# Kernel optimization log

Hardware: AMD Instinct MI355X
Metric: run time of the kernel (lower is better)

The kernel has to match this reference:

```python
import jax, jax.numpy as jnp
import numpy as np
import math

IMAGE_SIZE = 256
VIEWING_ANGLE = 30.0  # degrees
NEAR = 0.1
FAR = 100.0
CHUNK = 50


def _look_at(vertices):
    # nr.look_at with at=origin, up=+y, eye from viewing_angle (as in __init__)
    eye = jnp.array([0.0, 0.0, -(1.0 / math.tan(math.radians(VIEWING_ANGLE)) + 1.0)],
                    dtype=vertices.dtype)
    at = jnp.zeros(3, dtype=vertices.dtype)
    up = jnp.array([0.0, 1.0, 0.0], dtype=vertices.dtype)
    z = at - eye
    z = z / jnp.linalg.norm(z)
    x = jnp.cross(up, z)
    x = x / jnp.linalg.norm(x)
    y = jnp.cross(z, x)
    y = y / jnp.linalg.norm(y)
    R = jnp.stack([x, y, z])  # [3,3] rows = camera axes
    return (vertices - eye) @ R.T


def _perspective(v):
    # nr.perspective: x,y divided by z*tan(angle); z (camera depth) kept
    width = math.tan(math.radians(VIEWING_ANGLE))
    z = v[..., 2]
    zs = jnp.where(jnp.abs(z) < 1e-5, 1e-5, z)  # avoid div-by-zero for behind-camera verts
    return jnp.stack([v[..., 0] / (zs * width), v[..., 1] / (zs * width), z], axis=-1)


def reference(vertices, faces):
    """Renderer.forward(vertices, faces, mode='depth'):
    fill_back -> look_at -> perspective -> vertices_to_faces -> rasterize_depth.
    Returns depth image [B, H, W] (FAR where no face covers the pixel)."""
    B = vertices.shape[0]
    # fill_back: append faces with reversed vertex order
    faces2 = jnp.concatenate([faces, faces[:, :, ::-1]], axis=1)  # [B, 2F, 3]
    v_scr = _perspective(_look_at(vertices))                      # [B, V, 3]
    # vertices_to_faces gather
    fv = jax.vmap(lambda v, f: v[f])(v_scr, faces2)               # [B, 2F, 3, 3]
    F2 = fv.shape[1]
    nsteps = F2 // CHUNK
    fv = fv.reshape(B, nsteps, CHUNK, 3, 3).transpose(1, 0, 2, 3, 4)  # [S,B,C,3,3]

    is_ = IMAGE_SIZE
    p = (2.0 * jnp.arange(is_, dtype=vertices.dtype) + 1.0 - is_) / is_  # pixel centers in (-1,1)
    py, px = jnp.meshgrid(p, p, indexing='ij')  # [H,W]

    def step(buf, f):  # f: [B,C,3,3]; z-buffer min over this face chunk
        x = f[..., 0][..., None, None]  # [B,C,3,1,1]
        y = f[..., 1][..., None, None]
        z = f[..., 2]                   # [B,C,3] camera-space depth per vertex
        x0, x1, x2 = x[:, :, 0], x[:, :, 1], x[:, :, 2]
        y0, y1, y2 = y[:, :, 0], y[:, :, 1], y[:, :, 2]
        area = (x1 - x0) * (y2 - y0) - (x2 - x0) * (y1 - y0)  # [B,C,1,1] signed 2*area
        area_s = jnp.where(jnp.abs(area) < 1e-8, 1e-8, area)
        # screen-space barycentric weights (edge functions / area)
        w0 = ((x1 - px) * (y2 - py) - (x2 - px) * (y1 - py)) / area_s
        w1 = ((x2 - px) * (y0 - py) - (x0 - px) * (y2 - py)) / area_s
        w2 = 1.0 - w0 - w1
        zc = jnp.maximum(z, 1e-4)  # safe for masked-out faces only
        # perspective-correct depth: z = 1 / (w0/z0 + w1/z1 + w2/z2)
        inv_z = (w0 / zc[:, :, 0, None, None] + w1 / zc[:, :, 1, None, None]
                 + w2 / zc[:, :, 2, None, None])
        zp = 1.0 / jnp.maximum(inv_z, 1e-6)
        front = jnp.all(z > NEAR, axis=-1)[..., None, None]
        inside = (w0 >= 0) & (w1 >= 0) & (w2 >= 0) & (jnp.abs(area) > 1e-8)
        valid = inside & front & (zp > NEAR) & (zp < FAR)
        zp = jnp.where(valid, zp, FAR)
        return jnp.minimum(buf, jnp.min(zp, axis=1)), None

    buf0 = jnp.full((B, is_, is_), FAR, dtype=vertices.dtype)
    depth, _ = jax.lax.scan(step, buf0, fv)
    return depth


def setup_inputs() -> dict:
    key = jax.random.key(0)
    kv, kf = jax.random.split(key)
    B, NV, NF = 1, 2502, 5000
    # mesh roughly within the camera frustum (eye at z~-2.73 looking at origin)
    vertices = 0.35 * jax.random.normal(kv, (B, NV, 3), dtype=jnp.float32)
    faces = jax.random.randint(kf, (B, NF, 3), 0, NV, dtype=jnp.int32)
    return {"vertices": vertices, "faces": faces}
```

## Files before the change

kernel.cpp:

```cpp
#include <hip/hip_runtime.h>
#include <hip/hip_bf16.h>

#define IS 256
#define NEARV 0.1f
#define FARV 100.0f
#define NTX 16
#define NTILES 256
#define CAP 5120
#define CHK 32
#define BINTH 128
#define RBLOCKS 2048
#define RWAVES (RBLOCKS * 4)
#define MAXITEMS (NTILES * ((CAP + CHK - 1) / CHK))

__global__ void kprep(const float* __restrict__ verts, const int* __restrict__ faces,
                      float4* __restrict__ fd, unsigned int* __restrict__ zb,
                      int* __restrict__ count, int* __restrict__ nitems, int nf) {
    int i = blockIdx.x * 256 + threadIdx.x;
    zb[i] = 0x42C80000u;
    if (i < NTILES) count[i] = 0;
    if (i == NTILES) *nitems = 0;
    if (i >= nf) return;
    int i0 = faces[i * 3 + 0];
    int i1 = faces[i * 3 + 1];
    int i2 = faces[i * 3 + 2];
    float z0 = verts[i0 * 3 + 2] + 2.7320508075688772f;
    float z1 = verts[i1 * 3 + 2] + 2.7320508075688772f;
    float z2 = verts[i2 * 3 + 2] + 2.7320508075688772f;
    bool front = (z0 > NEARV) && (z1 > NEARV) && (z2 > NEARV);
    float zs0 = (fabsf(z0) < 1e-5f) ? 1e-5f : z0;
    float zs1 = (fabsf(z1) < 1e-5f) ? 1e-5f : z1;
    float zs2 = (fabsf(z2) < 1e-5f) ? 1e-5f : z2;
    float d0 = zs0 * 0.57735026918962576f;
    float d1 = zs1 * 0.57735026918962576f;
    float d2 = zs2 * 0.57735026918962576f;
    float x0 = verts[i0 * 3 + 0] / d0;
    float y0 = verts[i0 * 3 + 1] / d0;
    float x1 = verts[i1 * 3 + 0] / d1;
    float y1 = verts[i1 * 3 + 1] / d1;
    float x2 = verts[i2 * 3 + 0] / d2;
    float y2 = verts[i2 * 3 + 1] / d2;
    float area = (x1 - x0) * (y2 - y0) - (x2 - x0) * (y1 - y0);
    float4* o = fd + (size_t)i * 4;
    if (front && (fabsf(area) > 1e-8f)) {
        float xmin = fminf(x0, fminf(x1, x2));
        float xmax = fmaxf(x0, fmaxf(x1, x2));
        float ymin = fminf(y0, fminf(y1, y2));
        float ymax = fmaxf(y0, fmaxf(y1, y2));
        float ia = 1.0f / area;
        float iz0 = 1.0f / fmaxf(z0, 1e-4f);
        float iz1 = 1.0f / fmaxf(z1, 1e-4f);
        float iz2 = 1.0f / fmaxf(z2, 1e-4f);
        o[0] = make_float4(x0, y0, x1, y1);
        o[1] = make_float4(x2, y2, ia, iz0);
        o[2] = make_float4(iz1, iz2, 0.0f, 0.0f);
        o[3] = make_float4(xmin, ymin, xmax, ymax);
    } else {
        o[3] = make_float4(3.0e8f, 3.0e8f, -3.0e8f, -3.0e8f);
    }
}

__global__ void kbin(const float4* __restrict__ fd, int* __restrict__ count,
                     unsigned short* __restrict__ list, int nf) {
    __shared__ int scnt[NTILES];
    __shared__ int sbase[NTILES];
    const int tid = threadIdx.x;
    for (int t = tid; t < NTILES; t += BINTH) scnt[t] = 0;
    __syncthreads();
    const int f = blockIdx.x * BINTH + tid;
    int kx0 = 0, kx1 = -1, ky0 = 0, ky1 = -1;
    float4 bb = make_float4(0.f, 0.f, 0.f, 0.f);
    if (f < nf) {
        bb = fd[(size_t)f * 4 + 3];
        float tminx = fminf(fmaxf((bb.x * 256.0f + 225.0f) * (1.0f / 32.0f), -2.0f), 17.0f);
        float tmaxx = fminf(fmaxf((bb.z * 256.0f + 255.0f) * (1.0f / 32.0f), -2.0f), 17.0f);
        float tminy = fminf(fmaxf((bb.y * 256.0f + 225.0f) * (1.0f / 32.0f), -2.0f), 17.0f);
        float tmaxy = fminf(fmaxf((bb.w * 256.0f + 255.0f) * (1.0f / 32.0f), -2.0f), 17.0f);
        kx0 = max(0, (int)ceilf(tminx) - 1);
        kx1 = min(NTX - 1, (int)floorf(tmaxx) + 1);
        ky0 = max(0, (int)ceilf(tminy) - 1);
        ky1 = min(NTX - 1, (int)floorf(tmaxy) + 1);
    }
    for (int ky = ky0; ky <= ky1; ++ky) {
        float py_lo = (float)(32 * ky - 255) * (1.0f / 256.0f);
        float py_hi = (float)(32 * ky - 225) * (1.0f / 256.0f);
        if (!(bb.y <= py_hi && bb.w >= py_lo)) continue;
        for (int kx = kx0; kx <= kx1; ++kx) {
            float px_lo = (float)(32 * kx - 255) * (1.0f / 256.0f);
            float px_hi = (float)(32 * kx - 225) * (1.0f / 256.0f);
            if (bb.x <= px_hi && bb.z >= px_lo) atomicAdd(&scnt[ky * NTX + kx], 1);
        }
    }
    __syncthreads();
    for (int t = tid; t < NTILES; t += BINTH) {
        int c = scnt[t];
        sbase[t] = (c > 0) ? atomicAdd(&count[t], c) : 0;
        scnt[t] = 0;
    }
    __syncthreads();
    for (int ky = ky0; ky <= ky1; ++ky) {
        float py_lo = (float)(32 * ky - 255) * (1.0f / 256.0f);
        float py_hi = (float)(32 * ky - 225) * (1.0f / 256.0f);
        if (!(bb.y <= py_hi && bb.w >= py_lo)) continue;
        for (int kx = kx0; kx <= kx1; ++kx) {
            float px_lo = (float)(32 * kx - 255) * (1.0f / 256.0f);
            float px_hi = (float)(32 * kx - 225) * (1.0f / 256.0f);
            if (bb.x <= px_hi && bb.z >= px_lo) {
                int t = ky * NTX + kx;
                int slot = sbase[t] + atomicAdd(&scnt[t], 1);
                list[(size_t)t * CAP + slot] = (unsigned short)f;
            }
        }
    }
}

__global__ void kitems(const int* __restrict__ count, int* __restrict__ items,
                       int* __restrict__ nitems) {
    __shared__ int snch[NTILES];
    __shared__ int soff[NTILES];
    const int t = threadIdx.x;
    int c = count[t];
    snch[t] = (c + CHK - 1) / CHK;
    __syncthreads();
    if (t == 0) {
        int run = 0;
        for (int i = 0; i < NTILES; ++i) { soff[i] = run; run += snch[i]; }
        *nitems = run;
    }
    __syncthreads();
    int off = soff[t];
    int n = snch[t];
    for (int k = 0; k < n; ++k) items[off + k] = (t << 16) | k;
}

__launch_bounds__(256)
__global__ void kraster(const float4* __restrict__ fd, const unsigned short* __restrict__ list,
                        const int* __restrict__ count, const int* __restrict__ items,
                        const int* __restrict__ nitems, unsigned int* __restrict__ zb) {
    const int wid = blockIdx.x * 4 + (threadIdx.x >> 6);
    const int lane = threadIdx.x & 63;
    const int cx = lane & 15;
    const int ry = lane >> 4;
    const int ni = *nitems;

    for (int it = wid; it < ni; it += RWAVES) {
        const int pk = items[it];
        const int tile = pk >> 16;
        const int chunk = pk & 0xffff;
        const int bx = tile & 15;
        const int by = tile >> 4;
        const int j = bx * 16 + cx;
        const float px = ((float)(2 * j + 1) - 256.0f) * (1.0f / 256.0f);
        float py[4];
        int row[4];
#pragma unroll
        for (int r = 0; r < 4; ++r) {
            row[r] = by * 16 + ry + 4 * r;
            py[r] = ((float)(2 * row[r] + 1) - 256.0f) * (1.0f / 256.0f);
        }
        const int s = chunk * CHK;
        const int n = min(CHK, count[tile] - s);
        const unsigned short* lp = list + (size_t)tile * CAP + s;

        float mx[4] = {0.0f, 0.0f, 0.0f, 0.0f};

#pragma unroll 2
        for (int e = 0; e < n; ++e) {
            const int fidx = lp[e];
            const float4* p = fd + (size_t)fidx * 4;
            float4 a0 = p[0];
            float4 a1 = p[1];
            float4 a2 = p[2];
            float dx0 = a0.x - px, dx1 = a0.z - px, dx2 = a1.x - px;
#pragma unroll
            for (int r = 0; r < 4; ++r) {
                float dy0 = a0.y - py[r], dy1 = a0.w - py[r], dy2 = a1.y - py[r];
                float e0 = dx1 * dy2 - dx2 * dy1;
                float e1 = dx2 * dy0 - dx0 * dy2;
                float w0 = e0 * a1.z;
                float w1 = e1 * a1.z;
                float w2 = 1.0f - w0 - w1;
                float invz = w0 * a1.w + w1 * a2.x + w2 * a2.y;
                float invzc = fmaxf(invz, 1e-6f);
                bool ok = (w0 >= 0.0f) && (w1 >= 0.0f) && (w2 >= 0.0f) &&
                          (invzc < 10.0f) && (invzc > 0.01f);
                if (ok) mx[r] = fmaxf(mx[r], invzc);
            }
        }
#pragma unroll
        for (int r = 0; r < 4; ++r) {
            if (mx[r] > 0.0f) {
                float zp = 1.0f / mx[r];
                atomicMin(&zb[row[r] * IS + j], __float_as_uint(zp));
            }
        }
    }
}

extern "C" void kernel_launch(void* const* d_in, const int* in_sizes, int n_in,
                              void* d_out, int out_size, void* d_ws, size_t ws_size,
                              hipStream_t stream) {
    const float* verts = (const float*)d_in[0];
    const int* faces = (const int*)d_in[1];
    unsigned int* zb = (unsigned int*)d_out;

    const int nf = in_sizes[1] / 3;

    char* ws = (char*)d_ws;
    size_t off = 0;
    float4* fd = (float4*)(ws + off);            off += (size_t)nf * 64;
    off = (off + 255) & ~(size_t)255;
    int* count = (int*)(ws + off);               off += NTILES * 4;
    off = (off + 255) & ~(size_t)255;
    int* nitems = (int*)(ws + off);              off += 256;
    int* items = (int*)(ws + off);               off += (size_t)MAXITEMS * 4;
    off = (off + 255) & ~(size_t)255;
    unsigned short* list = (unsigned short*)(ws + off);

    kprep<<<(IS * IS) / 256, 256, 0, stream>>>(verts, faces, fd, zb, count, nitems, nf);
    kbin<<<(nf + BINTH - 1) / BINTH, BINTH, 0, stream>>>(fd, count, list, nf);
    kitems<<<1, 256, 0, stream>>>(count, items, nitems);
    kraster<<<RBLOCKS, 256, 0, stream>>>(fd, list, count, items, nitems, zb);
}
```

Before: 109.3 us.

## Store face data directly in tile bins and drop the item-list kernel

The binning kernel now writes each face's 48-byte setup record straight into per-tile bin slots, so the rasterizer streams contiguous records instead of indirecting through 16-bit face indices. The single-block kitems prefix kernel is removed. Rasterizer waves instead iterate over a fixed grid of tile×slot pairs, skewed across tiles, and skip empty slots. The launch is doubled to 4096 blocks. This removes one kernel launch plus a serial scan and the gather indirection, at the cost of much larger binning writes and many idle waves checking empty slots.

```diff
diff --git a/kernel.cpp b/kernel.cpp
--- a/kernel.cpp
+++ b/kernel.cpp
@@ -8,18 +8,18 @@
 #define NTILES 256
 #define CAP 5120
 #define CHK 32
+#define SLOTMAX (CAP / CHK)
+#define NSLOTS (NTILES * SLOTMAX)
 #define BINTH 128
-#define RBLOCKS 2048
+#define RBLOCKS 4096
 #define RWAVES (RBLOCKS * 4)
-#define MAXITEMS (NTILES * ((CAP + CHK - 1) / CHK))
 
 __global__ void kprep(const float* __restrict__ verts, const int* __restrict__ faces,
                       float4* __restrict__ fd, unsigned int* __restrict__ zb,
-                      int* __restrict__ count, int* __restrict__ nitems, int nf) {
+                      int* __restrict__ count, int nf) {
     int i = blockIdx.x * 256 + threadIdx.x;
     zb[i] = 0x42C80000u;
     if (i < NTILES) count[i] = 0;
-    if (i == NTILES) *nitems = 0;
     if (i >= nf) return;
     int i0 = faces[i * 3 + 0];
     int i1 = faces[i * 3 + 1];
@@ -61,7 +61,7 @@
 }
 
 __global__ void kbin(const float4* __restrict__ fd, int* __restrict__ count,
-                     unsigned short* __restrict__ list, int nf) {
+                     float4* __restrict__ list48, int nf) {
     __shared__ int scnt[NTILES];
     __shared__ int sbase[NTILES];
     const int tid = threadIdx.x;
@@ -98,6 +98,11 @@
         scnt[t] = 0;
     }
     __syncthreads();
+    float4 r0, r1, r2;
+    if (f < nf && ky1 >= ky0) {
+        const float4* p = fd + (size_t)f * 4;
+        r0 = p[0]; r1 = p[1]; r2 = p[2];
+    }
     for (int ky = ky0; ky <= ky1; ++ky) {
         float py_lo = (float)(32 * ky - 255) * (1.0f / 256.0f);
         float py_hi = (float)(32 * ky - 225) * (1.0f / 256.0f);
@@ -108,45 +113,28 @@
             if (bb.x <= px_hi && bb.z >= px_lo) {
                 int t = ky * NTX + kx;
                 int slot = sbase[t] + atomicAdd(&scnt[t], 1);
-                list[(size_t)t * CAP + slot] = (unsigned short)f;
+                float4* dst = list48 + ((size_t)t * CAP + slot) * 3;
+                dst[0] = r0; dst[1] = r1; dst[2] = r2;
             }
         }
     }
 }
 
-__global__ void kitems(const int* __restrict__ count, int* __restrict__ items,
-                       int* __restrict__ nitems) {
-    __shared__ int snch[NTILES];
-    __shared__ int soff[NTILES];
-    const int t = threadIdx.x;
-    int c = count[t];
-    snch[t] = (c + CHK - 1) / CHK;
-    __syncthreads();
-    if (t == 0) {
-        int run = 0;
-        for (int i = 0; i < NTILES; ++i) { soff[i] = run; run += snch[i]; }
-        *nitems = run;
-    }
-    __syncthreads();
-    int off = soff[t];
-    int n = snch[t];
-    for (int k = 0; k < n; ++k) items[off + k] = (t << 16) | k;
-}
-
 __launch_bounds__(256)
-__global__ void kraster(const float4* __restrict__ fd, const unsigned short* __restrict__ list,
-                        const int* __restrict__ count, const int* __restrict__ items,
-                        const int* __restrict__ nitems, unsigned int* __restrict__ zb) {
+__global__ void kraster(const float4* __restrict__ list48, const int* __restrict__ count,
+                        unsigned int* __restrict__ zb) {
     const int wid = blockIdx.x * 4 + (threadIdx.x >> 6);
     const int lane = threadIdx.x & 63;
     const int cx = lane & 15;
     const int ry = lane >> 4;
-    const int ni = *nitems;
-
-    for (int it = wid; it < ni; it += RWAVES) {
-        const int pk = items[it];
-        const int tile = pk >> 16;
-        const int chunk = pk & 0xffff;
+
+    for (int it = wid; it < NSLOTS; it += RWAVES) {
+        const int slot = it >> 8;
+        const int tile = (it + slot) & 255;
+        const int cnt = count[tile];
+        const int n = min(CHK, cnt - slot * CHK);
+        if (n <= 0) continue;
+
         const int bx = tile & 15;
         const int by = tile >> 4;
         const int j = bx * 16 + cx;
@@ -158,19 +146,15 @@
             row[r] = by * 16 + ry + 4 * r;
             py[r] = ((float)(2 * row[r] + 1) - 256.0f) * (1.0f / 256.0f);
         }
-        const int s = chunk * CHK;
-        const int n = min(CHK, count[tile] - s);
-        const unsigned short* lp = list + (size_t)tile * CAP + s;
+        const float4* base = list48 + ((size_t)tile * CAP + slot * CHK) * 3;
 
         float mx[4] = {0.0f, 0.0f, 0.0f, 0.0f};
 
 #pragma unroll 2
         for (int e = 0; e < n; ++e) {
-            const int fidx = lp[e];
-            const float4* p = fd + (size_t)fidx * 4;
-            float4 a0 = p[0];
-            float4 a1 = p[1];
-            float4 a2 = p[2];
+            float4 a0 = base[e * 3 + 0];
+            float4 a1 = base[e * 3 + 1];
+            float4 a2 = base[e * 3 + 2];
             float dx0 = a0.x - px, dx1 = a0.z - px, dx2 = a1.x - px;
 #pragma unroll
             for (int r = 0; r < 4; ++r) {
@@ -208,17 +192,13 @@
 
     char* ws = (char*)d_ws;
     size_t off = 0;
-    float4* fd = (float4*)(ws + off);            off += (size_t)nf * 64;
+    float4* fd = (float4*)(ws + off);    off += (size_t)nf * 64;
     off = (off + 255) & ~(size_t)255;
-    int* count = (int*)(ws + off);               off += NTILES * 4;
+    int* count = (int*)(ws + off);       off += NTILES * 4;
     off = (off + 255) & ~(size_t)255;
-    int* nitems = (int*)(ws + off);              off += 256;
-    int* items = (int*)(ws + off);               off += (size_t)MAXITEMS * 4;
-    off = (off + 255) & ~(size_t)255;
-    unsigned short* list = (unsigned short*)(ws + off);
-
-    kprep<<<(IS * IS) / 256, 256, 0, stream>>>(verts, faces, fd, zb, count, nitems, nf);
-    kbin<<<(nf + BINTH - 1) / BINTH, BINTH, 0, stream>>>(fd, count, list, nf);
-    kitems<<<1, 256, 0, stream>>>(count, items, nitems);
-    kraster<<<RBLOCKS, 256, 0, stream>>>(fd, list, count, items, nitems, zb);
-}
+    float4* list48 = (float4*)(ws + off);
+
+    kprep<<<(IS * IS) / 256, 256, 0, stream>>>(verts, faces, fd, zb, count, nf);
+    kbin<<<(nf + BINTH - 1) / BINTH, BINTH, 0, stream>>>(fd, count, list48, nf);
+    kraster<<<RBLOCKS, 256, 0, stream>>>(list48, count, zb);
+}
```

Result: slower. 126.5 us (+15.8%).
